# Optimization experiments

Hardware: AMD Instinct MI355X
Metric: run time of the kernel (lower is better)

The kernel has to match this reference:

```python
import jax, jax.numpy as jnp
from jax import lax
import numpy as np

EPS = 1e-3  # epsilon from __init__


def setup_inputs() -> dict:
    key = jax.random.key(0)
    k_x, k_m, k_v, k_p = jax.random.split(key, 4)
    B, C, H, W = 16, 64, 128, 128
    K = 8  # num_contexts
    x = jax.random.normal(k_x, (B, C, H, W), dtype=jnp.float32)
    # Parameters as initialized by reset_parameters():
    mean = jax.random.uniform(k_m, (K, 1), minval=-1.0, maxval=1.0, dtype=jnp.float32)
    variance = jax.random.uniform(k_v, (K, 1), minval=0.001, maxval=0.01, dtype=jnp.float32)
    p0 = jax.random.uniform(k_p, (K, 1), dtype=jnp.float32)
    prior = p0 / jnp.sum(p0, axis=0, keepdims=True)
    return {"x": x, "mean": mean, "variance": variance, "prior": prior}


def reference(x, mean, variance, prior):
    # Eval-mode forward of AdaptiveContextNorm (4D input path).
    mu = mean[:, 0]                      # (K,) scalar mean per context (expand over C is a broadcast)
    v = jax.nn.softplus(variance[:, 0])  # (K,)
    pr = jax.nn.softmax(prior[:, 0], axis=0)  # (K,)

    # Pass 1: mixture denominator. NOTE: faithful to source, the denominator
    # uses var WITHOUT +eps in the 4D path (ternary-precedence quirk), while
    # the numerator p_x_given_k uses (var + eps).
    def denom_step(acc, params):
        m, vv, pk = params
        return acc + pk * jnp.exp(-0.5 * ((x - m) / vv) ** 2), None

    denom, _ = lax.scan(denom_step, jnp.zeros_like(x), (mu, v, pr))

    # Pass 2: accumulate normalized output.
    def out_step(acc, params):
        m, vv, pk = params
        p_x_given_k = pk * jnp.exp(-0.5 * ((x - m) / (vv + EPS)) ** 2)
        tau_k = p_x_given_k / (denom + EPS)
        hat_x = (x - m) / jnp.sqrt(vv + EPS)
        return acc + tau_k / jnp.sqrt(pk + EPS) * hat_x, None

    out, _ = lax.scan(out_step, jnp.zeros_like(x), (mu, v, pr))
    return out
```

## Files before the change

### kernel.cpp

```cpp
#include <hip/hip_runtime.h>

#define ACN_EPS   0.001f
#define ACN_LOG2E 1.4426950408889634f
#define ACN_LN2   0.6931471805599453f

typedef float v4f __attribute__((ext_vector_type(4)));

__global__ void acn_setup(const float* __restrict__ mean,
                          const float* __restrict__ variance,
                          const float* __restrict__ prior,
                          float* __restrict__ P) {
    int lane = threadIdx.x;
    int k = lane & 7;
    float m  = mean[k];
    float va = variance[k];
    float p0 = prior[k];

    float v = logf(1.0f + expf(va));
    float mx = p0;
    for (int off = 1; off < 8; off <<= 1) mx = fmaxf(mx, __shfl_xor(mx, off, 64));
    float e = expf(p0 - mx);
    float sum = e;
    for (int off = 1; off < 8; off <<= 1) sum += __shfl_xor(sum, off, 64);
    float pk = e / sum;

    float s1 = -0.5f * ACN_LOG2E / (v * v);
    float ve = v + ACN_EPS;
    float s2 = -0.5f * ACN_LOG2E / (ve * ve);
    float lp = log2f(pk);
    float C  = 1.0f / sqrtf((pk + ACN_EPS) * ve);
    float ds = (s2 - s1) * ACN_LN2;

    if (lane < 8) {
        P[k]      = m;
        P[8 + k]  = s1;
        P[16 + k] = lp;
        P[24 + k] = ds;
        P[32 + k] = C;
        P[40 + k] = C * 0.5f;
        P[48 + k] = C * (1.0f / 6.0f);
    }
}

__global__ __launch_bounds__(256) void acn_main(const v4f* __restrict__ x,
                                                v4f* __restrict__ out,
                                                const float* __restrict__ P,
                                                int n4) {
    float mu[8], s1[8], lp[8], ds[8], c0[8], c2[8], c3[8];
#pragma unroll
    for (int k = 0; k < 8; ++k) {
        mu[k] = P[k];
        s1[k] = P[8 + k];
        lp[k] = P[16 + k];
        ds[k] = P[24 + k];
        c0[k] = P[32 + k];
        c2[k] = P[40 + k];
        c3[k] = P[48 + k];
    }

    int idx    = blockIdx.x * blockDim.x + threadIdx.x;
    int stride = gridDim.x * blockDim.x;
    for (int i = idx; i < n4; i += stride) {
        v4f xv = x[i];
        float xs[4]    = {xv.x, xv.y, xv.z, xv.w};
        float denom[4] = {0.0f, 0.0f, 0.0f, 0.0f};
        float S[4]     = {0.0f, 0.0f, 0.0f, 0.0f};
#pragma unroll
        for (int k = 0; k < 8; ++k) {
#pragma unroll
            for (int j = 0; j < 4; ++j) {
                float d  = xs[j] - mu[k];
                float d2 = d * d;
                float E  = __builtin_amdgcn_exp2f(fmaf(s1[k], d2, lp[k]));
                denom[j] += E;
                float u  = ds[k] * d2;
                float q  = fmaf(u, c3[k], c2[k]);
                q        = fmaf(q, u, c0[k]);
                q        = fmaf(q, u, c0[k]);
                S[j]     = fmaf(E * d, q, S[j]);
            }
        }
        v4f ov;
        ov.x = S[0] * __builtin_amdgcn_rcpf(denom[0] + ACN_EPS);
        ov.y = S[1] * __builtin_amdgcn_rcpf(denom[1] + ACN_EPS);
        ov.z = S[2] * __builtin_amdgcn_rcpf(denom[2] + ACN_EPS);
        ov.w = S[3] * __builtin_amdgcn_rcpf(denom[3] + ACN_EPS);
        __builtin_nontemporal_store(ov, &out[i]);
    }
}

extern "C" void kernel_launch(void* const* d_in, const int* in_sizes, int n_in,
                              void* d_out, int out_size, void* d_ws, size_t ws_size,
                              hipStream_t stream) {
    const float* x        = (const float*)d_in[0];
    const float* mean     = (const float*)d_in[1];
    const float* variance = (const float*)d_in[2];
    const float* prior    = (const float*)d_in[3];
    float* out = (float*)d_out;
    float* P   = (float*)d_ws;

    acn_setup<<<1, 64, 0, stream>>>(mean, variance, prior, P);

    int n4 = out_size / 4;
    const int block = 256;
    const int grid  = 2048;
    acn_main<<<grid, block, 0, stream>>>((const v4f*)x, (v4f*)out, P, n4);
}
```

Baseline: 129.1 us.

## Use packed float2 math, drop cubic term, and software-prefetch loads

Rewrites the per-element math on two-wide float vectors so the compiler can emit packed FMA/mul/add instructions (v_pk_fma_f32 on CDNA). It truncates the polynomial correction factor from cubic to quadratic, removing one coefficient and one FMA per context. It also adds a fast path for the exact grid-size multiple that processes 8 vec4 items per thread with loads for the next pair issued before computing the current pair. This cuts ALU instruction count and hides memory latency, at the cost of slightly lower accuracy in the exp correction and more register pressure.

```diff
diff --git a/kernel.cpp b/kernel.cpp
--- a/kernel.cpp
+++ b/kernel.cpp
@@ -4,7 +4,10 @@
 #define ACN_LOG2E 1.4426950408889634f
 #define ACN_LN2   0.6931471805599453f
 
+typedef float v2f __attribute__((ext_vector_type(2)));
 typedef float v4f __attribute__((ext_vector_type(4)));
+
+__device__ __forceinline__ v2f splat2(float s) { v2f r = {s, s}; return r; }
 
 __global__ void acn_setup(const float* __restrict__ mean,
                           const float* __restrict__ variance,
@@ -38,15 +41,51 @@
         P[24 + k] = ds;
         P[32 + k] = C;
         P[40 + k] = C * 0.5f;
-        P[48 + k] = C * (1.0f / 6.0f);
     }
+}
+
+__device__ __forceinline__ v2f acn_v2(v2f X,
+                                      const float* mu, const float* s1,
+                                      const float* lp, const float* ds,
+                                      const float* c0, const float* c2) {
+    v2f den = {0.0f, 0.0f};
+    v2f S   = {0.0f, 0.0f};
+#pragma unroll
+    for (int k = 0; k < 8; ++k) {
+        v2f d   = X - splat2(mu[k]);
+        v2f d2  = d * d;
+        v2f arg = __builtin_elementwise_fma(splat2(s1[k]), d2, splat2(lp[k]));
+        v2f E;
+        E.x = __builtin_amdgcn_exp2f(arg.x);
+        E.y = __builtin_amdgcn_exp2f(arg.y);
+        den += E;
+        v2f u = splat2(ds[k]) * d2;
+        v2f q = __builtin_elementwise_fma(u, splat2(c2[k]), splat2(c0[k]));
+        q     = __builtin_elementwise_fma(q, u, splat2(c0[k]));
+        S     = __builtin_elementwise_fma(E * d, q, S);
+    }
+    v2f r;
+    r.x = S.x * __builtin_amdgcn_rcpf(den.x + ACN_EPS);
+    r.y = S.y * __builtin_amdgcn_rcpf(den.y + ACN_EPS);
+    return r;
+}
+
+__device__ __forceinline__ v4f acn_v4(v4f X,
+                                      const float* mu, const float* s1,
+                                      const float* lp, const float* ds,
+                                      const float* c0, const float* c2) {
+    v2f lo = {X.x, X.y}, hi = {X.z, X.w};
+    v2f rl = acn_v2(lo, mu, s1, lp, ds, c0, c2);
+    v2f rh = acn_v2(hi, mu, s1, lp, ds, c0, c2);
+    v4f r = {rl.x, rl.y, rh.x, rh.y};
+    return r;
 }
 
 __global__ __launch_bounds__(256) void acn_main(const v4f* __restrict__ x,
                                                 v4f* __restrict__ out,
                                                 const float* __restrict__ P,
                                                 int n4) {
-    float mu[8], s1[8], lp[8], ds[8], c0[8], c2[8], c3[8];
+    float mu[8], s1[8], lp[8], ds[8], c0[8], c2[8];
 #pragma unroll
     for (int k = 0; k < 8; ++k) {
         mu[k] = P[k];
@@ -55,37 +94,30 @@
         ds[k] = P[24 + k];
         c0[k] = P[32 + k];
         c2[k] = P[40 + k];
-        c3[k] = P[48 + k];
     }
 
-    int idx    = blockIdx.x * blockDim.x + threadIdx.x;
-    int stride = gridDim.x * blockDim.x;
-    for (int i = idx; i < n4; i += stride) {
-        v4f xv = x[i];
-        float xs[4]    = {xv.x, xv.y, xv.z, xv.w};
-        float denom[4] = {0.0f, 0.0f, 0.0f, 0.0f};
-        float S[4]     = {0.0f, 0.0f, 0.0f, 0.0f};
+    const int T   = gridDim.x * blockDim.x;
+    const int idx = blockIdx.x * blockDim.x + threadIdx.x;
+
+    if (n4 == 8 * T) {
+        v4f a = x[idx];
+        v4f b = x[idx + T];
 #pragma unroll
-        for (int k = 0; k < 8; ++k) {
-#pragma unroll
-            for (int j = 0; j < 4; ++j) {
-                float d  = xs[j] - mu[k];
-                float d2 = d * d;
-                float E  = __builtin_amdgcn_exp2f(fmaf(s1[k], d2, lp[k]));
-                denom[j] += E;
-                float u  = ds[k] * d2;
-                float q  = fmaf(u, c3[k], c2[k]);
-                q        = fmaf(q, u, c0[k]);
-                q        = fmaf(q, u, c0[k]);
-                S[j]     = fmaf(E * d, q, S[j]);
+        for (int c = 0; c < 4; ++c) {
+            const int i = idx + c * 2 * T;
+            v4f an, bn;
+            if (c < 3) {
+                an = x[i + 2 * T];
+                bn = x[i + 3 * T];
             }
+            __builtin_nontemporal_store(acn_v4(a, mu, s1, lp, ds, c0, c2), &out[i]);
+            __builtin_nontemporal_store(acn_v4(b, mu, s1, lp, ds, c0, c2), &out[i + T]);
+            if (c < 3) { a = an; b = bn; }
         }
-        v4f ov;
-        ov.x = S[0] * __builtin_amdgcn_rcpf(denom[0] + ACN_EPS);
-        ov.y = S[1] * __builtin_amdgcn_rcpf(denom[1] + ACN_EPS);
-        ov.z = S[2] * __builtin_amdgcn_rcpf(denom[2] + ACN_EPS);
-        ov.w = S[3] * __builtin_amdgcn_rcpf(denom[3] + ACN_EPS);
-        __builtin_nontemporal_store(ov, &out[i]);
+    } else {
+        for (int i = idx; i < n4; i += T) {
+            __builtin_nontemporal_store(acn_v4(x[i], mu, s1, lp, ds, c0, c2), &out[i]);
+        }
     }
 }
 
```

Result: faster. 123.8 us (-4.1%).
